# Kernel tuning notes

Measured on AMD Instinct MI355X. Metric: run time of the kernel, lower is better.

Reference implementation:

```python
import jax, jax.numpy as jnp
import numpy as np
import math

D_MODEL = 512
N_HEADS = 8
D_FF = 2048
TOP_FACTOR = 5
LN_EPS = 1e-5


def _layernorm(x, g, b):
    m = jnp.mean(x, axis=-1, keepdims=True)
    v = jnp.mean((x - m) ** 2, axis=-1, keepdims=True)
    return (x - m) / jnp.sqrt(v + LN_EPS) * g + b


def _prob_sparse_attn(q_in, k_in, v_in, wq, bq, wk, bk, wv, bv, wo, bo):
    # weights stored (in, out): y = x @ w + b  (equivalent to torch Linear)
    B, Lq, dm = q_in.shape
    Lk = k_in.shape[1]
    H, D = N_HEADS, dm // N_HEADS
    q = (q_in @ wq + bq).reshape(B, Lq, H, D).transpose(0, 2, 1, 3)  # (B,H,Lq,D)
    k = (k_in @ wk + bk).reshape(B, Lk, H, D).transpose(0, 2, 1, 3)
    v = (v_in @ wv + bv).reshape(B, Lk, H, D).transpose(0, 2, 1, 3)

    qn = q / jnp.linalg.norm(q, axis=-1, keepdims=True)
    kn = k / jnp.linalg.norm(k, axis=-1, keepdims=True)
    # full cosine-similarity matrix, reduced to a row mean (as in the original)
    scores_all = jnp.einsum('bhqd,bhkd->bhqk', qn, kn)
    mean_scores = scores_all.mean(axis=-1)  # (B,H,Lq)

    u = max(1, Lq // TOP_FACTOR)
    _, top_idx = jax.lax.top_k(mean_scores, u)  # (B,H,u)

    q_sel = jnp.take_along_axis(q, top_idx[..., None], axis=2)  # (B,H,u,D)
    scores = jnp.einsum('bhud,bhkd->bhuk', q_sel, k) / math.sqrt(D)
    attn = jax.nn.softmax(scores, axis=-1)
    ctx_sel = jnp.einsum('bhuk,bhkd->bhud', attn, v)  # (B,H,u,D)

    b_ix = jnp.arange(B)[:, None, None]
    h_ix = jnp.arange(H)[None, :, None]
    context = jnp.zeros((B, H, Lq, D), dtype=q.dtype).at[b_ix, h_ix, top_idx].set(ctx_sel)
    out = context.transpose(0, 2, 1, 3).reshape(B, Lq, dm)
    return out @ wo + bo


def _decoder_layer(x, enc_out, p):
    xn = _layernorm(x, p['ln1_g'], p['ln1_b'])
    x = x + _prob_sparse_attn(xn, xn, xn, p['sa_wq'], p['sa_bq'], p['sa_wk'], p['sa_bk'],
                              p['sa_wv'], p['sa_bv'], p['sa_wo'], p['sa_bo'])
    xn = _layernorm(x, p['ln2_g'], p['ln2_b'])
    x = x + _prob_sparse_attn(xn, enc_out, enc_out, p['ca_wq'], p['ca_bq'], p['ca_wk'], p['ca_bk'],
                              p['ca_wv'], p['ca_bv'], p['ca_wo'], p['ca_bo'])
    xn = _layernorm(x, p['ln3_g'], p['ln3_b'])
    h = jax.nn.relu(xn @ p['ff_w1'] + p['ff_b1'])
    return x + (h @ p['ff_w2'] + p['ff_b2'])


def setup_inputs() -> dict:
    key = jax.random.key(0)
    ks = iter(jax.random.split(key, 32))
    B, L = 2, 2048
    dm, dff = D_MODEL, D_FF
    s = 1.0 / math.sqrt(dm)
    inp = {
        'x': jax.random.normal(next(ks), (B, L, dm), jnp.float32),
        'enc_out': jax.random.normal(next(ks), (B, L, dm), jnp.float32),
    }
    for pre in ('sa', 'ca'):
        for nm in ('wq', 'wk', 'wv', 'wo'):
            inp[f'{pre}_{nm}'] = jax.random.normal(next(ks), (dm, dm), jnp.float32) * s
            inp[f'{pre}_{nm[1:] and "b" + nm[1:]}'] = jnp.zeros((dm,), jnp.float32)
    inp['ff_w1'] = jax.random.normal(next(ks), (dm, dff), jnp.float32) * s
    inp['ff_b1'] = jnp.zeros((dff,), jnp.float32)
    inp['ff_w2'] = jax.random.normal(next(ks), (dff, dm), jnp.float32) / math.sqrt(dff)
    inp['ff_b2'] = jnp.zeros((dm,), jnp.float32)
    for i in (1, 2, 3):
        inp[f'ln{i}_g'] = jnp.ones((dm,), jnp.float32)
        inp[f'ln{i}_b'] = jnp.zeros((dm,), jnp.float32)
    return inp


def reference(x, enc_out,
              sa_wq, sa_bq, sa_wk, sa_bk, sa_wv, sa_bv, sa_wo, sa_bo,
              ca_wq, ca_bq, ca_wk, ca_bk, ca_wv, ca_bv, ca_wo, ca_bo,
              ff_w1, ff_b1, ff_w2, ff_b2,
              ln1_g, ln1_b, ln2_g, ln2_b, ln3_g, ln3_b):
    p = dict(sa_wq=sa_wq, sa_bq=sa_bq, sa_wk=sa_wk, sa_bk=sa_bk, sa_wv=sa_wv, sa_bv=sa_bv,
             sa_wo=sa_wo, sa_bo=sa_bo, ca_wq=ca_wq, ca_bq=ca_bq, ca_wk=ca_wk, ca_bk=ca_bk,
             ca_wv=ca_wv, ca_bv=ca_bv, ca_wo=ca_wo, ca_bo=ca_bo,
             ff_w1=ff_w1, ff_b1=ff_b1, ff_w2=ff_w2, ff_b2=ff_b2,
             ln1_g=ln1_g, ln1_b=ln1_b, ln2_g=ln2_g, ln2_b=ln2_b, ln3_g=ln3_g, ln3_b=ln3_b)
    return _decoder_layer(x, enc_out, p)
```

## Files before the change

kernel.cpp:

```cpp
#include <hip/hip_runtime.h>

#define BB 2
#define LL 2048
#define DM 512
#define NH 8
#define DH 64
#define DFF 2048
#define UU 409
#define ROWS (BB*LL)
#define X_ELEMS 2097152
#define NCHUNK 8

typedef unsigned short u16;
typedef __attribute__((ext_vector_type(8))) short short8;
typedef __attribute__((ext_vector_type(4))) float floatx4;

#define G_TOTAL 38200000
__device__ float g_buf[G_TOTAL];
__device__ int   g_isbf16;

#define A_Q     10495488
#define A_K     12592640
#define A_V     14689792
#define A_MKN   25175552
#define A_MS    25176576
#define A_RANK  25209344
#define A_PARTK 25242112
#define A_LIST  25274880
#define A_PO    25281536
#define A_PML   29475840
#define A_CTXF  16786944
#define XN_H    16796672
#define XN_L    18893824
#define CTX_H   33573888
#define CTX_L   35671040
#define ENC_H   37768192
#define ENC_L   39865344
#define AH_H    41962496
#define KH16    59213824
#define KL16    61310976
#define VTH16   63408128
#define VTL16   65505280
#define WT_SAQKV 67864576
#define WT_SAO   69437440
#define WT_CAQ   69961728
#define WT_CAKV  70486016
#define WT_CAO   71534592
#define WT_W1    72058880
#define WT_W2    74156032

__constant__ int c_end[28] = {
    2097152, 4194304, 4456448, 4456960, 4719104, 4719616, 4981760, 4982272,
    5244416, 5244928, 5507072, 5507584, 5769728, 5770240, 6032384, 6032896,
    6295040, 6295552, 7344128, 7346176, 8394752, 8395264, 8395776, 8396288,
    8396800, 8397312, 8397824, 8398336
};
__constant__ int sm_idx[16] = {3,5,7,9,11,13,15,17,19,21,22,23,24,25,26,27};
__constant__ int sm_cum[16] = {64,128,192,256,320,384,448,512,768,832,896,960,1024,1088,1152,1216};
#define XG 262144
#define EG 262144
#define SG 1216

__device__ __forceinline__ float bf2f(u16 x) {
    union { unsigned int u; float f; } c; c.u = ((unsigned int)x) << 16; return c.f;
}
__device__ __forceinline__ u16 f2bf(float f) {
    union { float f; unsigned int u; } c; c.f = f;
    unsigned int u = c.u;
    return (u16)((u + 0x7FFFu + ((u >> 16) & 1u)) >> 16);
}

struct P28 { const void* p[28]; };
struct I3 { int v[3]; };

__constant__ int tj[10][6] = {
    {2,  WT_SAQKV, 0,    512,  786432, 8},
    {4,  WT_SAQKV, 512,  512,  786432, 8},
    {6,  WT_SAQKV, 1024, 512,  786432, 8},
    {8,  WT_SAO,   0,    512,  262144, 8},
    {10, WT_CAQ,   0,    512,  262144, 8},
    {12, WT_CAKV,  0,    512,  524288, 8},
    {14, WT_CAKV,  512,  512,  524288, 8},
    {16, WT_CAO,   0,    512,  262144, 8},
    {18, WT_W1,    0,    512, 1048576, 32},
    {20, WT_W2,    0,   2048, 1048576, 8},
};
__constant__ int tcum[10] = {64, 128, 192, 256, 320, 384, 448, 512, 768, 1024};
__global__ void prep_all(P28 ps) {
    const int f = (((const u16*)ps.p[22])[0] == 0x3F80u) ? 1 : 0;
    if (blockIdx.x == 0 && threadIdx.x == 0) g_isbf16 = f;
    u16* gb16 = (u16*)g_buf;
    if (blockIdx.x < 1024) {
        int bid = blockIdx.x;
        int j = 0;
        while (bid >= tcum[j]) j++;
        int t = bid - (j ? tcum[j - 1] : 0);
        int widx = tj[j][0], wt = tj[j][1], col0 = tj[j][2];
        int K = tj[j][3], lo = tj[j][4], txn = tj[j][5];
        int Nsrc = txn * 64;
        int n0 = (t % txn) * 64, k0 = (t / txn) * 64;
        __shared__ float tb[64][65];
        int c = threadIdx.x & 63, r0 = threadIdx.x >> 6;
        const void* W = ps.p[widx];
        u16* WTh = gb16 + wt;
        for (int i = 0; i < 16; i++) {
            int r = r0 + 4 * i;
            size_t src = (size_t)(k0 + r) * Nsrc + n0 + c;
            tb[r][c] = f ? bf2f(((const u16*)W)[src]) : ((const float*)W)[src];
        }
        __syncthreads();
        for (int i = 0; i < 16; i++) {
            int r = r0 + 4 * i;
            float v = tb[c][r];
            u16 hi = f2bf(v);
            size_t o = (size_t)(col0 + n0 + r) * K + k0 + c;
            WTh[o] = hi;
            WTh[lo + o] = f2bf(v - bf2f(hi));
        }
        return;
    }
    int stride = 2048 * blockDim.x;
    for (int g = (blockIdx.x - 1024) * blockDim.x + threadIdx.x; g < XG + EG + SG; g += stride) {
        if (g < XG) {
            int e = g * 8;
            if (f) {
                uint4 raw = ((const uint4*)ps.p[0])[g];
                const u16* rr = (const u16*)&raw;
                float v[8] __attribute__((aligned(16)));
#pragma unroll
                for (int i = 0; i < 8; i++) v[i] = bf2f(rr[i]);
                *(float4*)(g_buf + e) = ((const float4*)v)[0];
                *(float4*)(g_buf + e + 4) = ((const float4*)v)[1];
            } else {
                *(uint4*)(g_buf + e)     = ((const uint4*)ps.p[0])[g * 2];
                *(uint4*)(g_buf + e + 4) = ((const uint4*)ps.p[0])[g * 2 + 1];
            }
        } else if (g < XG + EG) {
            int gl = g - XG;
            int e = gl * 8;
            float v[8] __attribute__((aligned(16)));
            if (f) {
                uint4 raw = ((const uint4*)ps.p[1])[gl];
                const u16* rr = (const u16*)&raw;
#pragma unroll
                for (int i = 0; i < 8; i++) v[i] = bf2f(rr[i]);
            } else {
                *(float4*)(v)     = ((const float4*)ps.p[1])[gl * 2];
                *(float4*)(v + 4) = ((const float4*)ps.p[1])[gl * 2 + 1];
            }
            u16 hh[8] __attribute__((aligned(16)));
            u16 lo[8] __attribute__((aligned(16)));
#pragma unroll
            for (int i = 0; i < 8; i++) { u16 hi = f2bf(v[i]); hh[i] = hi; lo[i] = f2bf(v[i] - bf2f(hi)); }
            *(uint4*)(&gb16[ENC_H + e]) = *(const uint4*)hh;
            *(uint4*)(&gb16[ENC_L + e]) = *(const uint4*)lo;
        } else {
            int t = g - XG - EG;
            int si = 0;
            while (t >= sm_cum[si]) si++;
            int s = sm_idx[si];
            int gl = t - (si ? sm_cum[si - 1] : 0);
            int e = gl * 8;
            float* dst = g_buf + c_end[s - 1] + e;
            if (f) {
                uint4 raw = *(const uint4*)((const u16*)ps.p[s] + e);
                const u16* rr = (const u16*)&raw;
#pragma unroll
                for (int i = 0; i < 8; i++) dst[i] = bf2f(rr[i]);
            } else {
                *(uint4*)(dst)     = *(const uint4*)((const float*)ps.p[s] + e);
                *(uint4*)(dst + 4) = *(const uint4*)((const float*)ps.p[s] + e + 4);
            }
        }
    }
}

__global__ void lnorm_k(int x_off, int g_off, int b_off, int yh_u16, int yl_u16) {
    int row = blockIdx.x;
    int tid = threadIdx.x;
    const float* x = g_buf + x_off + (size_t)row * DM;
    float a = x[tid], c = x[tid + 256];
    float s1 = a + c, s2 = a * a + c * c;
    for (int o = 32; o > 0; o >>= 1) { s1 += __shfl_xor(s1, o); s2 += __shfl_xor(s2, o); }
    __shared__ float r1[4], r2[4];
    int wave = tid >> 6, lane = tid & 63;
    if (lane == 0) { r1[wave] = s1; r2[wave] = s2; }
    __syncthreads();
    s1 = r1[0] + r1[1] + r1[2] + r1[3];
    s2 = r2[0] + r2[1] + r2[2] + r2[3];
    float mean = s1 * (1.0f / DM);
    float var  = s2 * (1.0f / DM) - mean * mean;
    float rstd = rsqrtf(var + 1e-5f);
    const float* gg = g_buf + g_off;
    const float* bb = g_buf + b_off;
    u16* yh = ((u16*)g_buf) + yh_u16 + (size_t)row * DM;
    u16* yl = ((u16*)g_buf) + yl_u16 + (size_t)row * DM;
    float v1 = (a - mean) * rstd * gg[tid]       + bb[tid];
    float v2 = (c - mean) * rstd * gg[tid + 256] + bb[tid + 256];
    u16 h1 = f2bf(v1), h2 = f2bf(v2);
    yh[tid] = h1;       yl[tid] = f2bf(v1 - bf2f(h1));
    yh[tid + 256] = h2; yl[tid + 256] = f2bf(v2 - bf2f(h2));
}

template<int WM, bool SPLIT, bool SEC, bool RELU, bool RESID, bool FINAL, bool OUTH>
__global__ void mgemm_k(I3 a_offs, I3 splt, I3 alz, int wt_u16_off, I3 boffs, int resid_off,
                        int out_off, void* __restrict__ dext, int M, int N, int K) {
    constexpr int BT_M = WM * 32;
    constexpr int A4 = BT_M * 4;
    __shared__ u16 Ash[BT_M * 40];
    __shared__ u16 Asl[SPLIT ? BT_M * 40 : 8];
    __shared__ u16 Bsh[128 * 40];
    __shared__ u16 Bsl[SPLIT ? 128 * 40 : 8];
    int sec_blk = SEC ? ((blockIdx.x * 128) >> 9) : 0;
    const u16* Ah = ((const u16*)g_buf) + a_offs.v[sec_blk];
    const u16* Al = Ah + (size_t)M * K;
    const u16* WTh = ((const u16*)g_buf) + wt_u16_off;
    const u16* WTl = WTh + (size_t)N * K;
    const int isbf = g_isbf16;
    const bool use_al = SPLIT && splt.v[sec_blk] && !(alz.v[sec_blk] && isbf);
    const bool use_bl = SPLIT && splt.v[sec_blk] && !isbf;
    int tid = threadIdx.x;
    int lane = tid & 63, wid = tid >> 6;
    int wm = wid >> 1, wn = wid & 1;
    int quad = lane >> 4, l15 = lane & 15;
    int m0 = blockIdx.y * BT_M, n0 = blockIdx.x * 128;
    floatx4 acc[WM][4];
#pragma unroll
    for (int i = 0; i < WM; i++)
#pragma unroll
        for (int j = 0; j < 4; j++) acc[i][j] = (floatx4){0.f, 0.f, 0.f, 0.f};
    for (int k0 = 0; k0 < K; k0 += 32) {
#pragma unroll
        for (int i = 0; i < (A4 + 255) / 256; i++) {
            int idx8 = tid + 256 * i;
            if (A4 % 256 == 0 || idx8 < A4) {
                int r = idx8 >> 2, c8 = (idx8 & 3) * 8;
                *(uint4*)(&Ash[r * 40 + c8]) = *(const uint4*)(Ah + (size_t)(m0 + r) * K + k0 + c8);
                if (SPLIT && use_al)
                    *(uint4*)(&Asl[r * 40 + c8]) = *(const uint4*)(Al + (size_t)(m0 + r) * K + k0 + c8);
            }
        }
#pragma unroll
        for (int i = 0; i < 2; i++) {
            int idx8 = tid + 256 * i;
            int r = idx8 >> 2, c8 = (idx8 & 3) * 8;
            *(uint4*)(&Bsh[r * 40 + c8]) = *(const uint4*)(WTh + (size_t)(n0 + r) * K + k0 + c8);
            if (SPLIT && use_bl)
                *(uint4*)(&Bsl[r * 40 + c8]) = *(const uint4*)(WTl + (size_t)(n0 + r) * K + k0 + c8);
        }
        __syncthreads();
        short8 ah[WM], bh[4], al[WM], bl[4];
#pragma unroll
        for (int i = 0; i < WM; i++) {
            int ro = (wm * WM * 16 + i * 16 + l15) * 40 + quad * 8;
            ah[i] = *(const short8*)(&Ash[ro]);
            if (SPLIT && use_al) al[i] = *(const short8*)(&Asl[ro]);
        }
#pragma unroll
        for (int j = 0; j < 4; j++) {
            int ro = (wn * 64 + j * 16 + l15) * 40 + quad * 8;
            bh[j] = *(const short8*)(&Bsh[ro]);
            if (SPLIT && use_bl) bl[j] = *(const short8*)(&Bsl[ro]);
        }
#pragma unroll
        for (int i = 0; i < WM; i++)
#pragma unroll
            for (int j = 0; j < 4; j++) {
                acc[i][j] = __builtin_amdgcn_mfma_f32_16x16x32_bf16(ah[i], bh[j], acc[i][j], 0, 0, 0);
                if constexpr (SPLIT) {
                    if (use_bl)
                        acc[i][j] = __builtin_amdgcn_mfma_f32_16x16x32_bf16(ah[i], bl[j], acc[i][j], 0, 0, 0);
                    if (use_al)
                        acc[i][j] = __builtin_amdgcn_mfma_f32_16x16x32_bf16(al[i], bh[j], acc[i][j], 0, 0, 0);
                }
            }
        __syncthreads();
    }
#pragma unroll
    for (int i = 0; i < WM; i++)
#pragma unroll
        for (int j = 0; j < 4; j++)
#pragma unroll
            for (int r = 0; r < 4; r++) {
                int row = m0 + wm * WM * 16 + i * 16 + quad * 4 + r;
                int col = n0 + wn * 64 + j * 16 + l15;
                int sec = SEC ? (col >> 9) : 0;
                int ci  = SEC ? (col & 511) : col;
                float v = acc[i][j][r] + g_buf[boffs.v[sec] + ci];
                if (RELU) v = fmaxf(v, 0.f);
                if (RESID) v += g_buf[resid_off + (size_t)row * N + col];
                if (FINAL) {
                    if (g_isbf16) ((u16*)dext)[(size_t)row * N + col] = f2bf(v);
                    else          ((float*)dext)[(size_t)row * N + col] = v;
                } else if (OUTH) {
                    ((u16*)g_buf)[out_off + (size_t)row * N + col] = f2bf(v);
                } else if (SEC) {
                    g_buf[out_off + ((size_t)sec * ROWS + row) * 512 + ci] = v;
                } else {
                    g_buf[out_off + (size_t)row * N + col] = v;
                }
            }
}

__global__ void meankn_p1(int k_off, int part_off) {
    int bh = blockIdx.x >> 5, chunk = blockIdx.x & 31;
    int b = bh >> 3, h = bh & 7;
    int wave = threadIdx.x >> 6, lane = threadIdx.x & 63;
    const float* base = g_buf + k_off + (size_t)b * LL * DM + (size_t)h * DH + lane;
    float acc = 0.f;
    for (int t = 0; t < 16; t++) {
        int j = chunk * 64 + wave * 16 + t;
        float kv = base[(size_t)j * DM];
        float s = kv * kv;
        for (int o = 32; o > 0; o >>= 1) s += __shfl_xor(s, o);
        acc += kv / sqrtf(fmaxf(s, 1e-30f));
    }
    __shared__ float red[4][64];
    red[wave][lane] = acc;
    __syncthreads();
    if (threadIdx.x < 64)
        g_buf[part_off + (size_t)blockIdx.x * 64 + threadIdx.x] =
            red[0][threadIdx.x] + red[1][threadIdx.x] + red[2][threadIdx.x] + red[3][threadIdx.x];
}

__global__ void mscore_k(int q_off, int part_off, int ms_off) {
    int bh = blockIdx.y, b = bh >> 3, h = bh & 7;
    int tid = threadIdx.x;
    __shared__ float mk[64];
    if (tid < 64) {
        float s = 0.f;
        for (int c = 0; c < 32; c++) s += g_buf[part_off + (size_t)(bh * 32 + c) * 64 + tid];
        mk[tid] = s * (1.0f / LL);
    }
    __syncthreads();
    int w = tid >> 6, lane = tid & 63;
    float m = mk[lane];
#pragma unroll
    for (int it = 0; it < 8; it++) {
        int row = blockIdx.x * 32 + it * 4 + w;
        float qv = g_buf[q_off + ((size_t)b * LL + row) * DM + h * DH + lane];
        float s = qv * qv, d = qv * m;
        for (int o = 32; o > 0; o >>= 1) { s += __shfl_xor(s, o); d += __shfl_xor(d, o); }
        if (lane == 0) g_buf[ms_off + bh * LL + row] = d / sqrtf(fmaxf(s, 1e-30f));
    }
}

__global__ void topsel_k(int ms_off, int list_off, int rank_off, int u) {
    __shared__ float s[LL];
    int bh = blockIdx.y, chunk = blockIdx.x;
    for (int i = threadIdx.x; i < LL; i += 256) s[i] = g_buf[ms_off + bh * LL + i];
    __syncthreads();
    int il = threadIdx.x >> 2;
    int i = chunk * 64 + il;
    int jq = threadIdx.x & 3;
    float si = s[i];
    int cnt = 0;
    for (int t = 0; t < 512; t++) {
        int j = jq * 512 + t;
        float sj = s[j];
        cnt += (sj > si) || (sj == si && j < i);
    }
    cnt += __shfl_xor(cnt, 1);
    cnt += __shfl_xor(cnt, 2);
    if (jq == 0) {
        int* list = (int*)(g_buf + list_off);
        int* rank = (int*)(g_buf + rank_off);
        if (cnt < u) { list[bh * 416 + cnt] = i; rank[bh * LL + i] = cnt; }
        else rank[bh * LL + i] = -1;
    }
}

template<bool LO>
__global__ void kvprep_k(int k_off, int v_off) {
    int bh = blockIdx.y, b = bh >> 3, h = bh & 7;
    int tok0 = blockIdx.x * 64;
    int tid = threadIdx.x;
    __shared__ float vt[64][68];
    u16* gb16 = (u16*)g_buf;
    int tok = tid >> 2, dq = (tid & 3) * 16;
    const float* kp = g_buf + k_off + ((size_t)(b * LL + tok0 + tok)) * DM + h * DH + dq;
    const float* vp = g_buf + v_off + ((size_t)(b * LL + tok0 + tok)) * DM + h * DH + dq;
    float kv[16] __attribute__((aligned(16)));
#pragma unroll
    for (int i = 0; i < 4; i++) *(float4*)(kv + 4 * i) = *(const float4*)(kp + 4 * i);
    u16 hh[16] __attribute__((aligned(16)));
    u16 lo[16] __attribute__((aligned(16)));
#pragma unroll
    for (int i = 0; i < 16; i++) { hh[i] = f2bf(kv[i]); if (LO) lo[i] = f2bf(kv[i] - bf2f(hh[i])); }
    size_t ko = ((size_t)(bh * LL + tok0 + tok)) * DH + dq;
    *(uint4*)(gb16 + KH16 + ko)     = ((const uint4*)hh)[0];
    *(uint4*)(gb16 + KH16 + ko + 8) = ((const uint4*)hh)[1];
    if (LO) {
        *(uint4*)(gb16 + KL16 + ko)     = ((const uint4*)lo)[0];
        *(uint4*)(gb16 + KL16 + ko + 8) = ((const uint4*)lo)[1];
    }
#pragma unroll
    for (int i = 0; i < 4; i++) *(float4*)(&vt[tok][dq + 4 * i]) = *(const float4*)(vp + 4 * i);
    __syncthreads();
    int d = tid >> 2, tq = (tid & 3) * 16;
    float vv[16];
#pragma unroll
    for (int i = 0; i < 16; i++) vv[i] = vt[tq + i][d];
#pragma unroll
    for (int i = 0; i < 16; i++) { hh[i] = f2bf(vv[i]); if (LO) lo[i] = f2bf(vv[i] - bf2f(hh[i])); }
    size_t vo = ((size_t)(bh * DH + d)) * LL + tok0 + tq;
    *(uint4*)(gb16 + VTH16 + vo)     = ((const uint4*)hh)[0];
    *(uint4*)(gb16 + VTH16 + vo + 8) = ((const uint4*)hh)[1];
    if (LO) {
        *(uint4*)(gb16 + VTL16 + vo)     = ((const uint4*)lo)[0];
        *(uint4*)(gb16 + VTL16 + vo + 8) = ((const uint4*)lo)[1];
    }
}

template<bool S3>
__global__ __launch_bounds__(256) void attn_flash(int q_off, int kh_off, int kl_off,
        int vth_off, int vtl_off, int list_off, int po_off, int pml_off, int u) {
    int bh = blockIdx.y, b = bh >> 3, h = bh & 7;
    int chunk = blockIdx.z;
    int tid = threadIdx.x, lane = tid & 63, w = tid >> 6;
    int quad = lane >> 4, l15 = lane & 15;
    const int* list = (const int*)(g_buf + list_off);

    short8 qh[2][2], ql[2][2];
#pragma unroll
    for (int g = 0; g < 2; g++) {
        int slot_q = blockIdx.x * 128 + w * 32 + g * 16 + l15;
        int qidx = list[bh * 416 + (slot_q < u ? slot_q : u - 1)];
        const float* qp = g_buf + q_off + ((size_t)b * LL + qidx) * DM + h * DH;
#pragma unroll
        for (int d2 = 0; d2 < 2; d2++) {
            float v[8] __attribute__((aligned(16)));
            *(float4*)(v)     = *(const float4*)(qp + d2 * 32 + quad * 8);
            *(float4*)(v + 4) = *(const float4*)(qp + d2 * 32 + quad * 8 + 4);
            u16 hh[8] __attribute__((aligned(16)));
            u16 lo[8] __attribute__((aligned(16)));
#pragma unroll
            for (int j = 0; j < 8; j++) {
                float s = v[j] * 0.125f;
                u16 hi = f2bf(s); hh[j] = hi; lo[j] = f2bf(s - bf2f(hi));
            }
            qh[g][d2] = *(const short8*)hh; ql[g][d2] = *(const short8*)lo;
        }
    }

    __shared__ u16 Ksh[64 * 68];
    __shared__ u16 Ksl[S3 ? 64 * 68 : 8];
    __shared__ u16 Vth[64 * 68];
    __shared__ u16 Vtl[S3 ? 64 * 68 : 8];
    __shared__ float smbuf[4352];

    const u16* gb16 = (const u16*)g_buf;
    const u16* KHp = gb16 + kh_off + (size_t)bh * LL * DH;
    const u16* KLp = gb16 + kl_off + (size_t)bh * LL * DH;
    const u16* VHp = gb16 + vth_off + (size_t)bh * DH * LL;
    const u16* VLp = gb16 + vtl_off + (size_t)bh * DH * LL;
    int r8 = tid >> 3;
    int gg = (tid & 7) * 8;

    uint4 pre[S3 ? 8 : 4];
    auto issue = [&](int row0) {
#pragma unroll
        for (int it = 0; it < 2; ++it) {
            int r = r8 + 32 * it;
            pre[it * (S3 ? 4 : 2) + 0] = *(const uint4*)(KHp + (size_t)(row0 + r) * DH + gg);
            pre[it * (S3 ? 4 : 2) + 1] = *(const uint4*)(VHp + (size_t)r * LL + row0 + gg);
            if constexpr (S3) {
                pre[it * 4 + 2] = *(const uint4*)(KLp + (size_t)(row0 + r) * DH + gg);
                pre[it * 4 + 3] = *(const uint4*)(VLp + (size_t)r * LL + row0 + gg);
            }
        }
    };
    auto commit = [&]() {
#pragma unroll
        for (int it = 0; it < 2; ++it) {
            int r = r8 + 32 * it;
            *(uint4*)(&Ksh[r * 68 + gg]) = pre[it * (S3 ? 4 : 2) + 0];
            *(uint4*)(&Vth[r * 68 + gg]) = pre[it * (S3 ? 4 : 2) + 1];
            if constexpr (S3) {
                *(uint4*)(&Ksl[r * 68 + gg]) = pre[it * 4 + 2];
                *(uint4*)(&Vtl[r * 68 + gg]) = pre[it * 4 + 3];
            }
        }
    };

    float m_run[2][4], l_run[2][4];
    floatx4 acc_o[2][4];
#pragma unroll
    for (int g = 0; g < 2; g++)
#pragma unroll
        for (int r = 0; r < 4; r++) {
            m_run[g][r] = -3.0e38f; l_run[g][r] = 0.f;
            acc_o[g][r] = (floatx4){0.f, 0.f, 0.f, 0.f};
        }

    issue(chunk * 256);
    for (int kt = 0; kt < 4; ++kt) {
        __syncthreads();
        commit();
        if (kt < 3) issue(chunk * 256 + (kt + 1) * 64);
        __syncthreads();
        float* ps = smbuf + w * 1088;
#pragma unroll
        for (int g = 0; g < 2; g++) {
            floatx4 sacc[4];
#pragma unroll
            for (int t = 0; t < 4; t++) {
                sacc[t] = (floatx4){0.f, 0.f, 0.f, 0.f};
#pragma unroll
                for (int d2 = 0; d2 < 2; d2++) {
                    int ro = (t * 16 + l15) * 68 + d2 * 32 + quad * 8;
                    short8 kh = *(const short8*)(&Ksh[ro]);
                    sacc[t] = __builtin_amdgcn_mfma_f32_16x16x32_bf16(qh[g][d2], kh, sacc[t], 0, 0, 0);
                    sacc[t] = __builtin_amdgcn_mfma_f32_16x16x32_bf16(ql[g][d2], kh, sacc[t], 0, 0, 0);
                    if constexpr (S3) {
                        short8 kl = *(const short8*)(&Ksl[ro]);
                        sacc[t] = __builtin_amdgcn_mfma_f32_16x16x32_bf16(qh[g][d2], kl, sacc[t], 0, 0, 0);
                    }
                }
            }
            float alpha[4];
#pragma unroll
            for (int r = 0; r < 4; r++) {
                float mx = fmaxf(fmaxf(sacc[0][r], sacc[1][r]), fmaxf(sacc[2][r], sacc[3][r]));
                for (int o = 1; o < 16; o <<= 1) mx = fmaxf(mx, __shfl_xor(mx, o));
                float mn = fmaxf(m_run[g][r], mx);
                alpha[r] = __expf(m_run[g][r] - mn);
                m_run[g][r] = mn;
                float ls = 0.f;
#pragma unroll
                for (int t = 0; t < 4; t++) {
                    float p = __expf(sacc[t][r] - mn);
                    sacc[t][r] = p;
                    ls += p;
                }
                for (int o = 1; o < 16; o <<= 1) ls += __shfl_xor(ls, o);
                l_run[g][r] = l_run[g][r] * alpha[r] + ls;
            }
#pragma unroll
            for (int t = 0; t < 4; t++)
#pragma unroll
                for (int r = 0; r < 4; r++)
                    ps[(quad * 4 + r) * 68 + t * 16 + l15] = sacc[t][r];
#pragma unroll
            for (int j = 0; j < 4; j++)
#pragma unroll
                for (int r = 0; r < 4; r++) acc_o[g][j][r] *= alpha[r];
#pragma unroll
            for (int s2 = 0; s2 < 2; s2++) {
                float pv[8] __attribute__((aligned(16)));
                *(float4*)(pv)     = *(const float4*)(&ps[l15 * 68 + s2 * 32 + quad * 8]);
                *(float4*)(pv + 4) = *(const float4*)(&ps[l15 * 68 + s2 * 32 + quad * 8 + 4]);
                u16 ph[8] __attribute__((aligned(16)));
                u16 pl[8] __attribute__((aligned(16)));
#pragma unroll
                for (int j = 0; j < 8; j++) { u16 hi = f2bf(pv[j]); ph[j] = hi; pl[j] = f2bf(pv[j] - bf2f(hi)); }
                short8 phv = *(const short8*)ph, plv = *(const short8*)pl;
#pragma unroll
                for (int j = 0; j < 4; j++) {
                    int ro = (j * 16 + l15) * 68 + s2 * 32 + quad * 8;
                    short8 vh = *(const short8*)(&Vth[ro]);
                    acc_o[g][j] = __builtin_amdgcn_mfma_f32_16x16x32_bf16(phv, vh, acc_o[g][j], 0, 0, 0);
                    acc_o[g][j] = __builtin_amdgcn_mfma_f32_16x16x32_bf16(plv, vh, acc_o[g][j], 0, 0, 0);
                    if constexpr (S3) {
                        short8 vl = *(const short8*)(&Vtl[ro]);
                        acc_o[g][j] = __builtin_amdgcn_mfma_f32_16x16x32_bf16(phv, vl, acc_o[g][j], 0, 0, 0);
                    }
                }
            }
        }
    }
#pragma unroll
    for (int g = 0; g < 2; g++)
#pragma unroll
        for (int r = 0; r < 4; r++) {
            int slot = blockIdx.x * 128 + w * 32 + g * 16 + quad * 4 + r;
            if (slot >= u) continue;
            size_t rec = ((size_t)(bh * NCHUNK + chunk)) * 512 + slot;
            float* po = g_buf + po_off + rec * 64;
#pragma unroll
            for (int j = 0; j < 4; j++) po[j * 16 + l15] = acc_o[g][j][r];
            if (l15 == 0) {
                float* pml = g_buf + pml_off + rec * 2;
                pml[0] = m_run[g][r]; pml[1] = l_run[g][r];
            }
        }
}

__global__ void attn_combine(int po_off, int pml_off, int rank_off, int u) {
    int bh = blockIdx.y;
    int b = bh >> 3, h = bh & 7;
    int tid = threadIdx.x;
    int qi = tid >> 4;
    int kb = tid & 15;
    int ds = kb * 4;
    int row = blockIdx.x * 16 + qi;
    int rank = ((const int*)(g_buf + rank_off))[bh * LL + row];
    size_t idx = ((size_t)b * LL + row) * DM + h * DH + ds;
    if (rank < 0) {
        ushort4 z = {0, 0, 0, 0};
        *(ushort4*)(((u16*)g_buf) + CTX_H + idx) = z;
        *(ushort4*)(((u16*)g_buf) + CTX_L + idx) = z;
        return;
    }
    float m = -3.0e38f;
#pragma unroll
    for (int c = 0; c < NCHUNK; c++)
        m = fmaxf(m, g_buf[pml_off + (((size_t)(bh * NCHUNK + c)) * 512 + rank) * 2]);
    float l = 0.f, O0 = 0.f, O1 = 0.f, O2 = 0.f, O3 = 0.f;
#pragma unroll
    for (int c = 0; c < NCHUNK; c++) {
        size_t rec = ((size_t)(bh * NCHUNK + c)) * 512 + rank;
        const float* pml = g_buf + pml_off + rec * 2;
        float a = __expf(pml[0] - m);
        l += a * pml[1];
        float4 o = *(const float4*)(g_buf + po_off + rec * 64 + ds);
        O0 += a * o.x; O1 += a * o.y; O2 += a * o.z; O3 += a * o.w;
    }
    float inv = 1.0f / l;
    float o0 = O0 * inv, o1 = O1 * inv, o2 = O2 * inv, o3 = O3 * inv;
    ushort4 hv, lv;
    hv.x = f2bf(o0); lv.x = f2bf(o0 - bf2f(hv.x));
    hv.y = f2bf(o1); lv.y = f2bf(o1 - bf2f(hv.y));
    hv.z = f2bf(o2); lv.z = f2bf(o2 - bf2f(hv.z));
    hv.w = f2bf(o3); lv.w = f2bf(o3 - bf2f(hv.w));
    *(ushort4*)(((u16*)g_buf) + CTX_H + idx) = hv;
    *(ushort4*)(((u16*)g_buf) + CTX_L + idx) = lv;
}

extern "C" void kernel_launch(void* const* d_in, const int* in_sizes, int n_in,
                              void* d_out, int out_size, void* d_ws, size_t ws_size,
                              hipStream_t stream) {
    static const int SZ[28] = {
        2097152, 2097152,
        262144, 512, 262144, 512, 262144, 512, 262144, 512,
        262144, 512, 262144, 512, 262144, 512, 262144, 512,
        1048576, 2048, 1048576, 512,
        512, 512, 512, 512, 512, 512
    };
    int OFF[28];
    int cur = 0;
    for (int i = 0; i < 28; i++) { OFF[i] = cur; cur += SZ[i]; }

    P28 ps;
    for (int i = 0; i < 28; i++) ps.p[i] = d_in[i];
    prep_all<<<3072, 256, 0, stream>>>(ps);

    auto select_attend = [&](bool sa) {
        if (sa) kvprep_k<true><<<dim3(32, 16), 256, 0, stream>>>(A_K, A_V);
        else    kvprep_k<false><<<dim3(32, 16), 256, 0, stream>>>(A_K, A_V);
        meankn_p1<<<16 * 32, 256, 0, stream>>>(A_K, A_PARTK);
        mscore_k<<<dim3(64, 16), 256, 0, stream>>>(A_Q, A_PARTK, A_MS);
        topsel_k<<<dim3(32, 16), 256, 0, stream>>>(A_MS, A_LIST, A_RANK, UU);
        if (sa)
            attn_flash<true><<<dim3(4, 16, NCHUNK), 256, 0, stream>>>(
                A_Q, KH16, KL16, VTH16, VTL16, A_LIST, A_PO, A_PML, UU);
        else
            attn_flash<false><<<dim3(4, 16, NCHUNK), 256, 0, stream>>>(
                A_Q, KH16, KL16, VTH16, VTL16, A_LIST, A_PO, A_PML, UU);
        attn_combine<<<dim3(128, 16), 256, 0, stream>>>(A_PO, A_PML, A_RANK, UU);
    };

    lnorm_k<<<ROWS, 256, 0, stream>>>(OFF[0], OFF[22], OFF[23], XN_H, XN_L);
    mgemm_k<2, true, true, false, false, false, false><<<dim3(12, 64), 256, 0, stream>>>(
        I3{{XN_H, XN_H, XN_H}}, I3{{1, 1, 1}}, I3{{0, 0, 0}},
        WT_SAQKV, I3{{OFF[3], OFF[5], OFF[7]}}, 0, A_Q, nullptr, ROWS, 1536, 512);
    select_attend(true);
    mgemm_k<1, true, false, false, true, false, false><<<dim3(4, 128), 256, 0, stream>>>(
        I3{{CTX_H, 0, 0}}, I3{{1, 0, 0}}, I3{{0, 0, 0}},
        WT_SAO, I3{{OFF[9], 0, 0}}, OFF[0], OFF[0], nullptr, ROWS, 512, 512);

    lnorm_k<<<ROWS, 256, 0, stream>>>(OFF[0], OFF[24], OFF[25], XN_H, XN_L);
    mgemm_k<1, true, false, false, false, false, false><<<dim3(4, 128), 256, 0, stream>>>(
        I3{{XN_H, 0, 0}}, I3{{1, 0, 0}}, I3{{0, 0, 0}},
        WT_CAQ, I3{{OFF[11], 0, 0}}, 0, A_Q, nullptr, ROWS, 512, 512);
    mgemm_k<2, true, true, false, false, false, false><<<dim3(8, 64), 256, 0, stream>>>(
        I3{{ENC_H, ENC_H, ENC_H}}, I3{{1, 0, 0}}, I3{{1, 0, 0}},
        WT_CAKV, I3{{OFF[13], OFF[15], 0}}, 0, A_K, nullptr, ROWS, 1024, 512);
    select_attend(false);
    mgemm_k<1, false, false, false, true, false, false><<<dim3(4, 128), 256, 0, stream>>>(
        I3{{CTX_H, 0, 0}}, I3{{0, 0, 0}}, I3{{0, 0, 0}},
        WT_CAO, I3{{OFF[17], 0, 0}}, OFF[0], OFF[0], nullptr, ROWS, 512, 512);

    lnorm_k<<<ROWS, 256, 0, stream>>>(OFF[0], OFF[26], OFF[27], XN_H, XN_L);
    mgemm_k<4, false, false, true, false, false, true><<<dim3(16, 32), 256, 0, stream>>>(
        I3{{XN_H, 0, 0}}, I3{{0, 0, 0}}, I3{{0, 0, 0}},
        WT_W1, I3{{OFF[19], 0, 0}}, 0, AH_H, nullptr, ROWS, 2048, 512);
    mgemm_k<1, false, false, false, true, true, false><<<dim3(4, 128), 256, 0, stream>>>(
        I3{{AH_H, 0, 0}}, I3{{0, 0, 0}}, I3{{0, 0, 0}},
        WT_W2, I3{{OFF[21], 0, 0}}, OFF[0], 0, d_out, ROWS, 512, 2048);
}
```

Before: 576.8 us.

## Split attention query tiles finer and shrink key tiles to raise occupancy

The sparse flash-attention kernel now gives each block 64 selected queries (16 per wave) instead of 128, and processes 32-key tiles over 8 iterations instead of 64-key tiles over 4. The grid becomes a flat 896 blocks (7 query tiles x 16 heads x 8 chunks), launch bounds request 4 blocks per CU, and shared memory per block shrinks. The aim is more blocks in flight to cover the 304 CUs and fewer registers per thread. In exchange there are more sync barriers per block and K/V tiles are loaded by more blocks.

```diff
diff --git a/kernel.cpp b/kernel.cpp
--- a/kernel.cpp
+++ b/kernel.cpp
@@ -413,18 +413,20 @@
 }
 
 template<bool S3>
-__global__ __launch_bounds__(256) void attn_flash(int q_off, int kh_off, int kl_off,
+__global__ __launch_bounds__(256, 4) void attn_flash(int q_off, int kh_off, int kl_off,
         int vth_off, int vtl_off, int list_off, int po_off, int pml_off, int u) {
-    int bh = blockIdx.y, b = bh >> 3, h = bh & 7;
-    int chunk = blockIdx.z;
+    int bid = blockIdx.x;
+    int grp = bid & 127;
+    int sxt = bid >> 7;
+    int bh = grp & 15, chunk = grp >> 4;
+    int b = bh >> 3, h = bh & 7;
     int tid = threadIdx.x, lane = tid & 63, w = tid >> 6;
     int quad = lane >> 4, l15 = lane & 15;
     const int* list = (const int*)(g_buf + list_off);
 
-    short8 qh[2][2], ql[2][2];
-#pragma unroll
-    for (int g = 0; g < 2; g++) {
-        int slot_q = blockIdx.x * 128 + w * 32 + g * 16 + l15;
+    short8 qh[2], ql[2];
+    {
+        int slot_q = sxt * 64 + w * 16 + l15;
         int qidx = list[bh * 416 + (slot_q < u ? slot_q : u - 1)];
         const float* qp = g_buf + q_off + ((size_t)b * LL + qidx) * DM + h * DH;
 #pragma unroll
@@ -439,151 +441,130 @@
                 float s = v[j] * 0.125f;
                 u16 hi = f2bf(s); hh[j] = hi; lo[j] = f2bf(s - bf2f(hi));
             }
-            qh[g][d2] = *(const short8*)hh; ql[g][d2] = *(const short8*)lo;
-        }
-    }
-
-    __shared__ u16 Ksh[64 * 68];
-    __shared__ u16 Ksl[S3 ? 64 * 68 : 8];
-    __shared__ u16 Vth[64 * 68];
-    __shared__ u16 Vtl[S3 ? 64 * 68 : 8];
-    __shared__ float smbuf[4352];
+            qh[d2] = *(const short8*)hh; ql[d2] = *(const short8*)lo;
+        }
+    }
+
+    __shared__ u16 Ksh[32 * 68];
+    __shared__ u16 Ksl[S3 ? 32 * 68 : 8];
+    __shared__ u16 Vth[64 * 36];
+    __shared__ u16 Vtl[S3 ? 64 * 36 : 8];
+    __shared__ float ps_all[4][16 * 36];
 
     const u16* gb16 = (const u16*)g_buf;
     const u16* KHp = gb16 + kh_off + (size_t)bh * LL * DH;
     const u16* KLp = gb16 + kl_off + (size_t)bh * LL * DH;
     const u16* VHp = gb16 + vth_off + (size_t)bh * DH * LL;
     const u16* VLp = gb16 + vtl_off + (size_t)bh * DH * LL;
-    int r8 = tid >> 3;
-    int gg = (tid & 7) * 8;
-
-    uint4 pre[S3 ? 8 : 4];
+    int krow = tid >> 3, kcol = (tid & 7) * 8;
+    int vd = tid >> 2, vcol = (tid & 3) * 8;
+
+    uint4 pre[S3 ? 4 : 2];
     auto issue = [&](int row0) {
-#pragma unroll
-        for (int it = 0; it < 2; ++it) {
-            int r = r8 + 32 * it;
-            pre[it * (S3 ? 4 : 2) + 0] = *(const uint4*)(KHp + (size_t)(row0 + r) * DH + gg);
-            pre[it * (S3 ? 4 : 2) + 1] = *(const uint4*)(VHp + (size_t)r * LL + row0 + gg);
-            if constexpr (S3) {
-                pre[it * 4 + 2] = *(const uint4*)(KLp + (size_t)(row0 + r) * DH + gg);
-                pre[it * 4 + 3] = *(const uint4*)(VLp + (size_t)r * LL + row0 + gg);
-            }
+        pre[0] = *(const uint4*)(KHp + (size_t)(row0 + krow) * DH + kcol);
+        pre[1] = *(const uint4*)(VHp + (size_t)vd * LL + row0 + vcol);
+        if constexpr (S3) {
+            pre[2] = *(const uint4*)(KLp + (size_t)(row0 + krow) * DH + kcol);
+            pre[3] = *(const uint4*)(VLp + (size_t)vd * LL + row0 + vcol);
         }
     };
     auto commit = [&]() {
-#pragma unroll
-        for (int it = 0; it < 2; ++it) {
-            int r = r8 + 32 * it;
-            *(uint4*)(&Ksh[r * 68 + gg]) = pre[it * (S3 ? 4 : 2) + 0];
-            *(uint4*)(&Vth[r * 68 + gg]) = pre[it * (S3 ? 4 : 2) + 1];
-            if constexpr (S3) {
-                *(uint4*)(&Ksl[r * 68 + gg]) = pre[it * 4 + 2];
-                *(uint4*)(&Vtl[r * 68 + gg]) = pre[it * 4 + 3];
-            }
+        *(uint4*)(&Ksh[krow * 68 + kcol]) = pre[0];
+        *(uint4*)(&Vth[vd * 36 + vcol]) = pre[1];
+        if constexpr (S3) {
+            *(uint4*)(&Ksl[krow * 68 + kcol]) = pre[2];
+            *(uint4*)(&Vtl[vd * 36 + vcol]) = pre[3];
         }
     };
 
-    float m_run[2][4], l_run[2][4];
-    floatx4 acc_o[2][4];
-#pragma unroll
-    for (int g = 0; g < 2; g++)
-#pragma unroll
-        for (int r = 0; r < 4; r++) {
-            m_run[g][r] = -3.0e38f; l_run[g][r] = 0.f;
-            acc_o[g][r] = (floatx4){0.f, 0.f, 0.f, 0.f};
-        }
+    float m_run[4], l_run[4];
+    floatx4 acc_o[4];
+#pragma unroll
+    for (int r = 0; r < 4; r++) {
+        m_run[r] = -3.0e38f; l_run[r] = 0.f;
+        acc_o[r] = (floatx4){0.f, 0.f, 0.f, 0.f};
+    }
 
     issue(chunk * 256);
-    for (int kt = 0; kt < 4; ++kt) {
+    for (int kt = 0; kt < 8; ++kt) {
         __syncthreads();
         commit();
-        if (kt < 3) issue(chunk * 256 + (kt + 1) * 64);
+        if (kt < 7) issue(chunk * 256 + (kt + 1) * 32);
         __syncthreads();
-        float* ps = smbuf + w * 1088;
-#pragma unroll
-        for (int g = 0; g < 2; g++) {
-            floatx4 sacc[4];
-#pragma unroll
-            for (int t = 0; t < 4; t++) {
-                sacc[t] = (floatx4){0.f, 0.f, 0.f, 0.f};
-#pragma unroll
-                for (int d2 = 0; d2 < 2; d2++) {
-                    int ro = (t * 16 + l15) * 68 + d2 * 32 + quad * 8;
-                    short8 kh = *(const short8*)(&Ksh[ro]);
-                    sacc[t] = __builtin_amdgcn_mfma_f32_16x16x32_bf16(qh[g][d2], kh, sacc[t], 0, 0, 0);
-                    sacc[t] = __builtin_amdgcn_mfma_f32_16x16x32_bf16(ql[g][d2], kh, sacc[t], 0, 0, 0);
-                    if constexpr (S3) {
-                        short8 kl = *(const short8*)(&Ksl[ro]);
-                        sacc[t] = __builtin_amdgcn_mfma_f32_16x16x32_bf16(qh[g][d2], kl, sacc[t], 0, 0, 0);
-                    }
+        float* ps = ps_all[w];
+        floatx4 sacc[2];
+#pragma unroll
+        for (int t = 0; t < 2; t++) {
+            sacc[t] = (floatx4){0.f, 0.f, 0.f, 0.f};
+#pragma unroll
+            for (int d2 = 0; d2 < 2; d2++) {
+                int ro = (t * 16 + l15) * 68 + d2 * 32 + quad * 8;
+                short8 kh = *(const short8*)(&Ksh[ro]);
+                sacc[t] = __builtin_amdgcn_mfma_f32_16x16x32_bf16(qh[d2], kh, sacc[t], 0, 0, 0);
+                sacc[t] = __builtin_amdgcn_mfma_f32_16x16x32_bf16(ql[d2], kh, sacc[t], 0, 0, 0);
+                if constexpr (S3) {
+                    short8 kl = *(const short8*)(&Ksl[ro]);
+                    sacc[t] = __builtin_amdgcn_mfma_f32_16x16x32_bf16(qh[d2], kl, sacc[t], 0, 0, 0);
                 }
             }
-            float alpha[4];
-#pragma unroll
-            for (int r = 0; r < 4; r++) {
-                float mx = fmaxf(fmaxf(sacc[0][r], sacc[1][r]), fmaxf(sacc[2][r], sacc[3][r]));
-                for (int o = 1; o < 16; o <<= 1) mx = fmaxf(mx, __shfl_xor(mx, o));
-                float mn = fmaxf(m_run[g][r], mx);
-                alpha[r] = __expf(m_run[g][r] - mn);
-                m_run[g][r] = mn;
-                float ls = 0.f;
-#pragma unroll
-                for (int t = 0; t < 4; t++) {
-                    float p = __expf(sacc[t][r] - mn);
-                    sacc[t][r] = p;
-                    ls += p;
-                }
-                for (int o = 1; o < 16; o <<= 1) ls += __shfl_xor(ls, o);
-                l_run[g][r] = l_run[g][r] * alpha[r] + ls;
-            }
-#pragma unroll
-            for (int t = 0; t < 4; t++)
-#pragma unroll
-                for (int r = 0; r < 4; r++)
-                    ps[(quad * 4 + r) * 68 + t * 16 + l15] = sacc[t][r];
-#pragma unroll
-            for (int j = 0; j < 4; j++)
-#pragma unroll
-                for (int r = 0; r < 4; r++) acc_o[g][j][r] *= alpha[r];
-#pragma unroll
-            for (int s2 = 0; s2 < 2; s2++) {
-                float pv[8] __attribute__((aligned(16)));
-                *(float4*)(pv)     = *(const float4*)(&ps[l15 * 68 + s2 * 32 + quad * 8]);
-                *(float4*)(pv + 4) = *(const float4*)(&ps[l15 * 68 + s2 * 32 + quad * 8 + 4]);
-                u16 ph[8] __attribute__((aligned(16)));
-                u16 pl[8] __attribute__((aligned(16)));
-#pragma unroll
-                for (int j = 0; j < 8; j++) { u16 hi = f2bf(pv[j]); ph[j] = hi; pl[j] = f2bf(pv[j] - bf2f(hi)); }
-                short8 phv = *(const short8*)ph, plv = *(const short8*)pl;
-#pragma unroll
-                for (int j = 0; j < 4; j++) {
-                    int ro = (j * 16 + l15) * 68 + s2 * 32 + quad * 8;
-                    short8 vh = *(const short8*)(&Vth[ro]);
-                    acc_o[g][j] = __builtin_amdgcn_mfma_f32_16x16x32_bf16(phv, vh, acc_o[g][j], 0, 0, 0);
-                    acc_o[g][j] = __builtin_amdgcn_mfma_f32_16x16x32_bf16(plv, vh, acc_o[g][j], 0, 0, 0);
-                    if constexpr (S3) {
-                        short8 vl = *(const short8*)(&Vtl[ro]);
-                        acc_o[g][j] = __builtin_amdgcn_mfma_f32_16x16x32_bf16(phv, vl, acc_o[g][j], 0, 0, 0);
-                    }
-                }
-            }
-        }
-    }
-#pragma unroll
-    for (int g = 0; g < 2; g++)
+        }
+        float alpha[4];
 #pragma unroll
         for (int r = 0; r < 4; r++) {
-            int slot = blockIdx.x * 128 + w * 32 + g * 16 + quad * 4 + r;
-            if (slot >= u) continue;
-            size_t rec = ((size_t)(bh * NCHUNK + chunk)) * 512 + slot;
-            float* po = g_buf + po_off + rec * 64;
-#pragma unroll
-            for (int j = 0; j < 4; j++) po[j * 16 + l15] = acc_o[g][j][r];
-            if (l15 == 0) {
-                float* pml = g_buf + pml_off + rec * 2;
-                pml[0] = m_run[g][r]; pml[1] = l_run[g][r];
-            }
-        }
+            float mx = fmaxf(sacc[0][r], sacc[1][r]);
+            for (int o = 1; o < 16; o <<= 1) mx = fmaxf(mx, __shfl_xor(mx, o));
+            float mn = fmaxf(m_run[r], mx);
+            alpha[r] = __expf(m_run[r] - mn);
+            m_run[r] = mn;
+            float p0 = __expf(sacc[0][r] - mn);
+            float p1 = __expf(sacc[1][r] - mn);
+            sacc[0][r] = p0; sacc[1][r] = p1;
+            float ls = p0 + p1;
+            for (int o = 1; o < 16; o <<= 1) ls += __shfl_xor(ls, o);
+            l_run[r] = l_run[r] * alpha[r] + ls;
+        }
+#pragma unroll
+        for (int t = 0; t < 2; t++)
+#pragma unroll
+            for (int r = 0; r < 4; r++)
+                ps[(quad * 4 + r) * 36 + t * 16 + l15] = sacc[t][r];
+#pragma unroll
+        for (int j = 0; j < 4; j++)
+#pragma unroll
+            for (int r = 0; r < 4; r++) acc_o[j][r] *= alpha[r];
+        float pv[8] __attribute__((aligned(16)));
+        *(float4*)(pv)     = *(const float4*)(&ps[l15 * 36 + quad * 8]);
+        *(float4*)(pv + 4) = *(const float4*)(&ps[l15 * 36 + quad * 8 + 4]);
+        u16 ph[8] __attribute__((aligned(16)));
+        u16 pl[8] __attribute__((aligned(16)));
+#pragma unroll
+        for (int j = 0; j < 8; j++) { u16 hi = f2bf(pv[j]); ph[j] = hi; pl[j] = f2bf(pv[j] - bf2f(hi)); }
+        short8 phv = *(const short8*)ph, plv = *(const short8*)pl;
+#pragma unroll
+        for (int j = 0; j < 4; j++) {
+            int ro = (j * 16 + l15) * 36 + quad * 8;
+            short8 vh = *(const short8*)(&Vth[ro]);
+            acc_o[j] = __builtin_amdgcn_mfma_f32_16x16x32_bf16(phv, vh, acc_o[j], 0, 0, 0);
+            acc_o[j] = __builtin_amdgcn_mfma_f32_16x16x32_bf16(plv, vh, acc_o[j], 0, 0, 0);
+            if constexpr (S3) {
+                short8 vl = *(const short8*)(&Vtl[ro]);
+                acc_o[j] = __builtin_amdgcn_mfma_f32_16x16x32_bf16(phv, vl, acc_o[j], 0, 0, 0);
+            }
+        }
+    }
+#pragma unroll
+    for (int r = 0; r < 4; r++) {
+        int slot = sxt * 64 + w * 16 + quad * 4 + r;
+        if (slot >= u) continue;
+        size_t rec = ((size_t)(bh * NCHUNK + chunk)) * 512 + slot;
+        float* po = g_buf + po_off + rec * 64;
+#pragma unroll
+        for (int j = 0; j < 4; j++) po[j * 16 + l15] = acc_o[j][r];
+        if (l15 == 0) {
+            float* pml = g_buf + pml_off + rec * 2;
+            pml[0] = m_run[r]; pml[1] = l_run[r];
+        }
+    }
 }
 
 __global__ void attn_combine(int po_off, int pml_off, int rank_off, int u) {
@@ -652,10 +633,10 @@
         mscore_k<<<dim3(64, 16), 256, 0, stream>>>(A_Q, A_PARTK, A_MS);
         topsel_k<<<dim3(32, 16), 256, 0, stream>>>(A_MS, A_LIST, A_RANK, UU);
         if (sa)
-            attn_flash<true><<<dim3(4, 16, NCHUNK), 256, 0, stream>>>(
+            attn_flash<true><<<896, 256, 0, stream>>>(
                 A_Q, KH16, KL16, VTH16, VTL16, A_LIST, A_PO, A_PML, UU);
         else
-            attn_flash<false><<<dim3(4, 16, NCHUNK), 256, 0, stream>>>(
+            attn_flash<false><<<896, 256, 0, stream>>>(
                 A_Q, KH16, KL16, VTH16, VTL16, A_LIST, A_PO, A_PML, UU);
         attn_combine<<<dim3(128, 16), 256, 0, stream>>>(A_PO, A_PML, A_RANK, UU);
     };
```

New measurement: 576.1 us. No clear change (-0.1%).
